# Optimization experiments

Measured on AMD Instinct MI355X. Metric: run time of the kernel, lower is better.

## Reference

```python
import jax, jax.numpy as jnp
import numpy as np

N = 8192      # num nodes
D = 128       # feature dim (input_dim)
E = 262144    # num edges (avg degree 32)
P = 4         # num perspectives (num_pers)
EPSILON = 0.3 # similarity threshold (args.epsilon)


def setup_inputs() -> dict:
    key = jax.random.key(0)
    k1, k2, k3, k4 = jax.random.split(key, 4)
    x = jax.random.normal(k1, (N, D), dtype=jnp.float32)
    ori_index = jax.random.randint(k2, (2, E), 0, N, dtype=jnp.int32)
    ori_weight = jax.random.uniform(k3, (E,), dtype=jnp.float32)
    w_pers = jax.random.normal(k4, (P, D), dtype=jnp.float32)  # weighted-cosine perspective weights
    return {"x": x, "ori_index": ori_index, "ori_weight": ori_weight, "w_pers": w_pers}


def reference(x, ori_index, ori_weight, w_pers):
    n = x.shape[0]
    # to_dense_adj: scatter edge weights into dense [N, N] adjacency (duplicate edges add)
    ori_g = jnp.zeros((n, n), dtype=x.dtype).at[ori_index[0], ori_index[1]].add(ori_weight)

    # GraphLearner (weighted multi-perspective cosine):
    # reweight features per perspective, L2-normalize, cosine sim, mean over perspectives
    xw = x[None, :, :] * w_pers[:, None, :]                              # [P, N, D]
    xn = xw / jnp.maximum(jnp.linalg.norm(xw, axis=-1, keepdims=True), 1e-12)
    sim = jnp.mean(jnp.einsum('pnd,pmd->pnm', xn, xn), axis=0)           # [N, N]
    # epsilon-thresholded learned graph
    sim_g = jnp.where(sim > EPSILON, sim, jnp.zeros_like(sim))

    # purified(sim, ori_g, epsilon): keep original edges where sim*ori_g > epsilon
    pur_g = jnp.where(sim * ori_g > EPSILON, ori_g, jnp.zeros_like(sim))
    new_g = pur_g + sim_g
    # dense_to_sparse has data-dependent output size; return the dense refined
    # adjacency (same information: edges = nonzero(new_g), weights = values).
    return new_g
```

## Files before the change

kernel.cpp:

```cpp
#include <hip/hip_runtime.h>
#include <hip/hip_bf16.h>
#include <stdint.h>

#define N_NODES 8192
#define DIM     128
#define KTOT    512
#define NEDGE   262144
#define EPS     0.3f
#define FIX_DELTA 0.0043f
#define FIX_CAP (1u << 19)
#define LCAP    512
#define HASH_BITS 19
#define HASH_SLOTS (1u << HASH_BITS)

typedef unsigned int u32;
typedef unsigned short u16;
typedef __attribute__((ext_vector_type(8))) short short8;
typedef __attribute__((ext_vector_type(4))) float float4v;

#define OFF_YF  0u
#define OFF_YB  16777216u
#define OFF_CTR 25165824u
#define OFF_HK  25166080u
#define OFF_HV  27263232u
#define OFF_FL  29360384u
#define OFF_UL  31457536u
#define ZERO_VEC4 262160u

__device__ __forceinline__ u16 f2bf(float f) {
    u32 b = __builtin_bit_cast(u32, f);
    b += 0x7fffu + ((b >> 16) & 1u);
    return (u16)(b >> 16);
}

__device__ __forceinline__ float wave_dot(const float* __restrict__ yf,
                                          u32 i, u32 j, int lane) {
    const float4v* ri = (const float4v*)(yf + (size_t)i * KTOT);
    const float4v* rj = (const float4v*)(yf + (size_t)j * KTOT);
    float4v p = ri[lane] * rj[lane] + ri[64 + lane] * rj[64 + lane];
    float s = p.x + p.y + p.z + p.w;
    #pragma unroll
    for (int o = 32; o >= 1; o >>= 1) s += __shfl_xor(s, o, 64);
    return s;
}

__device__ __forceinline__ bool is_edge(const u32* __restrict__ hkey, u32 cell) {
    u32 h = (cell * 2654435761u) >> (32 - HASH_BITS);
    while (true) {
        u32 k = hkey[h];
        if (k == 0u) return false;
        if (k == cell + 1u) return true;
        h = (h + 1u) & (HASH_SLOTS - 1u);
    }
}

__global__ void prep_y(const float* __restrict__ x, const float* __restrict__ wp,
                       float* __restrict__ yf, u16* __restrict__ yb,
                       uint4* __restrict__ zbase) {
    if (blockIdx.x >= 2048) {
        for (u32 idx = (blockIdx.x - 2048) * 256 + threadIdx.x; idx < ZERO_VEC4;
             idx += 512 * 256)
            zbase[idx] = make_uint4(0, 0, 0, 0);
        return;
    }
    int node = blockIdx.x * 4 + (threadIdx.x >> 6);
    int lane = threadIdx.x & 63;
    float x0 = x[node * DIM + lane];
    float x1 = x[node * DIM + lane + 64];
    for (int p = 0; p < 4; ++p) {
        float v0 = x0 * wp[p * DIM + lane];
        float v1 = x1 * wp[p * DIM + lane + 64];
        float ss = v0 * v0 + v1 * v1;
        #pragma unroll
        for (int o = 1; o < 64; o <<= 1) ss += __shfl_xor(ss, o, 64);
        float scale = 0.5f / fmaxf(sqrtf(ss), 1e-12f);
        float y0 = v0 * scale, y1 = v1 * scale;
        int base = node * KTOT + p * DIM;
        yf[base + lane] = y0;       yf[base + lane + 64] = y1;
        yb[base + lane] = f2bf(y0); yb[base + lane + 64] = f2bf(y1);
    }
}

__global__ void edge_insert(const int* __restrict__ idx, const float* __restrict__ w,
                            u32* __restrict__ hkey, float* __restrict__ hval,
                            u32* __restrict__ ucnt, u32* __restrict__ ulist) {
    int e = blockIdx.x * 256 + threadIdx.x;
    u32 cell = (u32)(idx[e] * N_NODES + idx[NEDGE + e]);
    float wv = w[e];
    u32 key = cell + 1u;
    u32 h = (cell * 2654435761u) >> (32 - HASH_BITS);
    while (true) {
        u32 old = atomicCAS(&hkey[h], 0u, key);
        if (old == 0u) { ulist[atomicAdd(ucnt, 1u)] = h; atomicAdd(&hval[h], wv); break; }
        if (old == key) { atomicAdd(&hval[h], wv); break; }
        h = (h + 1u) & (HASH_SLOTS - 1u);
    }
}

#define TM  128
#define BK  64
#define TLD 132

__global__ __launch_bounds__(512)
void gemm_sim(const u16* __restrict__ yb, const float* __restrict__ yf,
              float* __restrict__ out, u32* __restrict__ fcnt, u32* __restrict__ flst) {
    int r = blockIdx.y, c = blockIdx.x;
    int bm, bn;
    if (c < 64 - r) { bm = r;      bn = r + c; }
    else            { bm = 63 - r; bn = bm + (c - (64 - r)); }
    __shared__ __align__(16) char smem[64 * TLD * 4];
    u16* As = (u16*)smem;
    u16* Bs = As + TM * BK;
    float* tbuf = (float*)smem;
    __shared__ u32 s_cnt;
    __shared__ u32 s_list[LCAP];
    int tid = threadIdx.x;
    int lane = tid & 63, wid = tid >> 6;
    int wm = wid >> 1, wn = wid & 1;
    if (tid == 0) s_cnt = 0;

    float4v acc[2][4] = {};
    const u16* arow = yb + (size_t)(bm * TM) * KTOT;
    const u16* brow = yb + (size_t)(bn * TM) * KTOT;

    for (int kt = 0; kt < KTOT / BK; ++kt) {
        __syncthreads();
        #pragma unroll
        for (int q = 0; q < 2; ++q) {
            int cc = q * 512 + wid * 64 + lane;
            int row = cc >> 3;
            int kg = (cc & 7) ^ (row & 7);
            __builtin_amdgcn_global_load_lds(
                (const __attribute__((address_space(1))) void*)(const void*)(arow + (size_t)row * KTOT + kt * BK + kg * 8),
                (__attribute__((address_space(3))) void*)(void*)(As + (q * 512 + wid * 64) * 8),
                16, 0, 0);
            __builtin_amdgcn_global_load_lds(
                (const __attribute__((address_space(1))) void*)(const void*)(brow + (size_t)row * KTOT + kt * BK + kg * 8),
                (__attribute__((address_space(3))) void*)(void*)(Bs + (q * 512 + wid * 64) * 8),
                16, 0, 0);
        }
        __syncthreads();
        #pragma unroll
        for (int kk = 0; kk < 2; ++kk) {
            short8 af[2], bfr[4];
            int kg2 = kk * 4 + (lane >> 4);
            int mrow = wm * 32 + (lane & 15);
            int ncol = wn * 64 + (lane & 15);
            #pragma unroll
            for (int i = 0; i < 2; ++i) {
                int ra = mrow + i * 16;
                af[i] = *(const short8*)&As[ra * BK + ((kg2 ^ (ra & 7)) * 8)];
            }
            #pragma unroll
            for (int j = 0; j < 4; ++j) {
                int rb = ncol + j * 16;
                bfr[j] = *(const short8*)&Bs[rb * BK + ((kg2 ^ (rb & 7)) * 8)];
            }
            #pragma unroll
            for (int i = 0; i < 2; ++i)
                #pragma unroll
                for (int j = 0; j < 4; ++j)
                    acc[i][j] = __builtin_amdgcn_mfma_f32_16x16x32_bf16(
                        af[i], bfr[j], acc[i][j], 0, 0, 0);
        }
    }

    int quad = lane >> 4, lcol = lane & 15;
    #pragma unroll
    for (int i = 0; i < 2; ++i)
        #pragma unroll
        for (int j = 0; j < 4; ++j) {
            int gr0 = bm * TM + wm * 32 + i * 16 + quad * 4;
            int gc  = bn * TM + wn * 64 + j * 16 + lcol;
            #pragma unroll
            for (int rr = 0; rr < 4; ++rr) {
                float s = acc[i][j][rr];
                __builtin_nontemporal_store(s > EPS ? s : 0.f,
                                            &out[(size_t)(gr0 + rr) * N_NODES + gc]);
                if (fabsf(s - EPS) < FIX_DELTA) {
                    u32 cell = (u32)((gr0 + rr) * N_NODES + gc);
                    u32 li = atomicAdd(&s_cnt, 1u);
                    if (li < LCAP) s_list[li] = cell;
                    else { u32 g = atomicAdd(fcnt, 1u); if (g < FIX_CAP) flst[g] = cell; }
                }
            }
        }

    #pragma unroll
    for (int h = 0; h < 2; ++h) {
        __syncthreads();
        if (wn == h) {
            #pragma unroll
            for (int i = 0; i < 2; ++i) {
                int Lr = wm * 32 + i * 16 + quad * 4;
                #pragma unroll
                for (int j = 0; j < 4; ++j) {
                    int Lc = j * 16 + lcol;
                    *(float4v*)&tbuf[Lc * TLD + Lr] = acc[i][j];
                }
            }
        }
        __syncthreads();
        #pragma unroll
        for (int v = 0; v < 4; ++v) {
            int chunk = v * 512 + tid;
            int row = chunk >> 5, c4 = chunk & 31;
            float4v t = *(const float4v*)&tbuf[row * TLD + c4 * 4];
            float4v o;
            #pragma unroll
            for (int rr = 0; rr < 4; ++rr) o[rr] = t[rr] > EPS ? t[rr] : 0.f;
            __builtin_nontemporal_store(o,
                (float4v*)&out[(size_t)(bn * TM + h * 64 + row) * N_NODES + bm * TM + c4 * 4]);
        }
    }

    __syncthreads();
    u32 cnt = s_cnt < LCAP ? s_cnt : LCAP;
    for (u32 t = wid; t < cnt; t += 8) {
        u32 cell = s_list[t];
        u32 ii = cell >> 13, jj = cell & 8191u;
        float s = wave_dot(yf, ii, jj, lane);
        if (lane == 0) {
            float v = s > EPS ? s : 0.f;
            out[(size_t)ii * N_NODES + jj] = v;
            out[(size_t)jj * N_NODES + ii] = v;
        }
    }
}

__global__ void fix_and_edges(const float* __restrict__ yf,
                              const u32* __restrict__ fcnt, const u32* __restrict__ flst,
                              const u32* __restrict__ hkey, const float* __restrict__ hval,
                              const u32* __restrict__ ucnt, const u32* __restrict__ ulist,
                              float* __restrict__ out) {
    int lane = threadIdx.x & 63;
    if (blockIdx.x < 1024) {
        u32 count = *ucnt;
        u32 t = blockIdx.x * 256 + threadIdx.x;
        bool valid = t < count;
        u32 cell = 0; float a = 0.f, sg = 0.f; bool hard = false;
        if (valid) {
            u32 h = ulist[t];
            cell = hkey[h] - 1u;
            a = hval[h];
            sg = out[cell];
            hard = (a > 1.0f) ||
                   (fabsf(sg - EPS) < FIX_DELTA + 1e-6f) ||
                   (sg > 0.f && fabsf(sg * a - EPS) < FIX_DELTA * a + 1e-6f) ||
                   (sg == 0.f && a > 0.9855f);
            if (!hard && sg > 0.f)
                out[cell] = sg + ((sg * a > EPS) ? a : 0.f);
        }
        unsigned long long m = __ballot(hard);
        while (m) {
            int src = __builtin_ctzll(m);
            m &= m - 1;
            u32 cB = __shfl(cell, src, 64);
            float aB = __shfl(a, src, 64);
            float s = wave_dot(yf, cB >> 13, cB & 8191u, lane);
            if (lane == 0) {
                float v = s > EPS ? s : 0.f;
                if (s * aB > EPS) v += aB;
                out[cB] = v;
            }
        }
    } else {
        u32 count = *fcnt; if (count > FIX_CAP) count = FIX_CAP;
        u32 wv = (blockIdx.x - 1024) * 4 + (threadIdx.x >> 6);
        for (u32 t = wv; t < count; t += 64 * 4) {
            u32 cell = flst[t];
            u32 ii = cell >> 13, jj = cell & 8191u;
            float s = wave_dot(yf, ii, jj, lane);
            float v = s > EPS ? s : 0.f;
            u32 mir = jj * (u32)N_NODES + ii;
            if (lane == 0 && !is_edge(hkey, cell)) out[(size_t)ii * N_NODES + jj] = v;
            if (lane == 1 && !is_edge(hkey, mir))  out[(size_t)jj * N_NODES + ii] = v;
        }
    }
}

extern "C" void kernel_launch(void* const* d_in, const int* in_sizes, int n_in,
                              void* d_out, int out_size, void* d_ws, size_t ws_size,
                              hipStream_t stream) {
    const float* x  = (const float*)d_in[0];
    const int*   oi = (const int*)d_in[1];
    const float* ow = (const float*)d_in[2];
    const float* wp = (const float*)d_in[3];
    float* out = (float*)d_out;
    char* ws = (char*)d_ws;
    float* yf = (float*)(ws + OFF_YF);
    u16*   yb = (u16*)(ws + OFF_YB);
    u32*   fc = (u32*)(ws + OFF_CTR);
    u32*   uc = (u32*)(ws + OFF_CTR + 4);
    u32*   hk = (u32*)(ws + OFF_HK);
    float* hv = (float*)(ws + OFF_HV);
    u32*   fl = (u32*)(ws + OFF_FL);
    u32*   ul = (u32*)(ws + OFF_UL);

    prep_y<<<2560, 256, 0, stream>>>(x, wp, yf, yb, (uint4*)(ws + OFF_CTR));
    edge_insert<<<NEDGE / 256, 256, 0, stream>>>(oi, ow, hk, hv, uc, ul);
    gemm_sim<<<dim3(65, 32), 512, 0, stream>>>(yb, yf, out, fc, fl);
    fix_and_edges<<<1088, 256, 0, stream>>>(yf, fc, fl, hk, hv, uc, ul, out);
}
```

Measured before the change: 424.4 us.

## Fuse near-threshold fixes and edge merging into the GEMM epilogue via per-tile edge buckets

Edges are bucketed by the upper-triangular 128x128 tile they fall in during hash insertion, and the GEMM block that owns that tile now applies the edge merge and exact-fp32 recomputes itself. Near-threshold cells are recomputed in-wave through a ballot loop instead of being queued to a global list. This removes the separate fix_and_edges launch and its global fix list. In exchange the GEMM epilogue gets longer, and every block scans the whole overflow list. Edges in the mirrored lower tile must be read after both triangle writes by the same block, which the bucketing by the symmetric tile ensures.

Measured after the change: 429.0 us. Within noise of the previous version (+1.1%).

```diff
diff --git a/kernel.cpp b/kernel.cpp
--- a/kernel.cpp
+++ b/kernel.cpp
@@ -8,10 +8,11 @@
 #define NEDGE   262144
 #define EPS     0.3f
 #define FIX_DELTA 0.0043f
-#define FIX_CAP (1u << 19)
-#define LCAP    512
 #define HASH_BITS 19
 #define HASH_SLOTS (1u << HASH_BITS)
+#define NTRI    2080
+#define TRI_CAP 376
+#define OCAP    131072
 
 typedef unsigned int u32;
 typedef unsigned short u16;
@@ -21,11 +22,12 @@
 #define OFF_YF  0u
 #define OFF_YB  16777216u
 #define OFF_CTR 25165824u
-#define OFF_HK  25166080u
-#define OFF_HV  27263232u
-#define OFF_FL  29360384u
-#define OFF_UL  31457536u
-#define ZERO_VEC4 262160u
+#define OFF_BC  25166080u
+#define OFF_HK  25174528u
+#define OFF_HV  27271680u
+#define OFF_OL  29368832u
+#define OFF_BL  29893120u
+#define ZERO_VEC4 262688u
 
 __device__ __forceinline__ u16 f2bf(float f) {
     u32 b = __builtin_bit_cast(u32, f);
@@ -44,14 +46,10 @@
     return s;
 }
 
-__device__ __forceinline__ bool is_edge(const u32* __restrict__ hkey, u32 cell) {
-    u32 h = (cell * 2654435761u) >> (32 - HASH_BITS);
-    while (true) {
-        u32 k = hkey[h];
-        if (k == 0u) return false;
-        if (k == cell + 1u) return true;
-        h = (h + 1u) & (HASH_SLOTS - 1u);
-    }
+__device__ __forceinline__ u32 tri_of(u32 ti, u32 tj) {
+    u32 bm = ti < tj ? ti : tj;
+    u32 bn = ti < tj ? tj : ti;
+    return bm * (129u - bm) / 2u + (bn - bm);
 }
 
 __global__ void prep_y(const float* __restrict__ x, const float* __restrict__ wp,
@@ -83,15 +81,24 @@
 
 __global__ void edge_insert(const int* __restrict__ idx, const float* __restrict__ w,
                             u32* __restrict__ hkey, float* __restrict__ hval,
-                            u32* __restrict__ ucnt, u32* __restrict__ ulist) {
+                            u32* __restrict__ bcnt, u32* __restrict__ blist,
+                            u32* __restrict__ ocnt, u32* __restrict__ olist) {
     int e = blockIdx.x * 256 + threadIdx.x;
-    u32 cell = (u32)(idx[e] * N_NODES + idx[NEDGE + e]);
+    u32 i = (u32)idx[e], j = (u32)idx[NEDGE + e];
+    u32 cell = i * (u32)N_NODES + j;
     float wv = w[e];
     u32 key = cell + 1u;
     u32 h = (cell * 2654435761u) >> (32 - HASH_BITS);
     while (true) {
         u32 old = atomicCAS(&hkey[h], 0u, key);
-        if (old == 0u) { ulist[atomicAdd(ucnt, 1u)] = h; atomicAdd(&hval[h], wv); break; }
+        if (old == 0u) {
+            u32 tri = tri_of(i >> 7, j >> 7);
+            u32 bi = atomicAdd(&bcnt[tri], 1u);
+            if (bi < TRI_CAP) blist[tri * TRI_CAP + bi] = h;
+            else { u32 g = atomicAdd(ocnt, 1u); if (g < OCAP) olist[g] = h; }
+            atomicAdd(&hval[h], wv);
+            break;
+        }
         if (old == key) { atomicAdd(&hval[h], wv); break; }
         h = (h + 1u) & (HASH_SLOTS - 1u);
     }
@@ -103,7 +110,10 @@
 
 __global__ __launch_bounds__(512)
 void gemm_sim(const u16* __restrict__ yb, const float* __restrict__ yf,
-              float* __restrict__ out, u32* __restrict__ fcnt, u32* __restrict__ flst) {
+              float* __restrict__ out,
+              const u32* __restrict__ hkey, const float* __restrict__ hval,
+              const u32* __restrict__ bcnt, const u32* __restrict__ blist,
+              const u32* __restrict__ ocnt, const u32* __restrict__ olist) {
     int r = blockIdx.y, c = blockIdx.x;
     int bm, bn;
     if (c < 64 - r) { bm = r;      bn = r + c; }
@@ -112,12 +122,9 @@
     u16* As = (u16*)smem;
     u16* Bs = As + TM * BK;
     float* tbuf = (float*)smem;
-    __shared__ u32 s_cnt;
-    __shared__ u32 s_list[LCAP];
     int tid = threadIdx.x;
     int lane = tid & 63, wid = tid >> 6;
     int wm = wid >> 1, wn = wid & 1;
-    if (tid == 0) s_cnt = 0;
 
     float4v acc[2][4] = {};
     const u16* arow = yb + (size_t)(bm * TM) * KTOT;
@@ -177,12 +184,6 @@
                 float s = acc[i][j][rr];
                 __builtin_nontemporal_store(s > EPS ? s : 0.f,
                                             &out[(size_t)(gr0 + rr) * N_NODES + gc]);
-                if (fabsf(s - EPS) < FIX_DELTA) {
-                    u32 cell = (u32)((gr0 + rr) * N_NODES + gc);
-                    u32 li = atomicAdd(&s_cnt, 1u);
-                    if (li < LCAP) s_list[li] = cell;
-                    else { u32 g = atomicAdd(fcnt, 1u); if (g < FIX_CAP) flst[g] = cell; }
-                }
             }
         }
 
@@ -215,66 +216,96 @@
     }
 
     __syncthreads();
-    u32 cnt = s_cnt < LCAP ? s_cnt : LCAP;
-    for (u32 t = wid; t < cnt; t += 8) {
-        u32 cell = s_list[t];
-        u32 ii = cell >> 13, jj = cell & 8191u;
-        float s = wave_dot(yf, ii, jj, lane);
-        if (lane == 0) {
-            float v = s > EPS ? s : 0.f;
-            out[(size_t)ii * N_NODES + jj] = v;
-            out[(size_t)jj * N_NODES + ii] = v;
-        }
-    }
-}
-
-__global__ void fix_and_edges(const float* __restrict__ yf,
-                              const u32* __restrict__ fcnt, const u32* __restrict__ flst,
-                              const u32* __restrict__ hkey, const float* __restrict__ hval,
-                              const u32* __restrict__ ucnt, const u32* __restrict__ ulist,
-                              float* __restrict__ out) {
-    int lane = threadIdx.x & 63;
-    if (blockIdx.x < 1024) {
-        u32 count = *ucnt;
-        u32 t = blockIdx.x * 256 + threadIdx.x;
-        bool valid = t < count;
-        u32 cell = 0; float a = 0.f, sg = 0.f; bool hard = false;
+
+    #pragma unroll
+    for (int i = 0; i < 2; ++i)
+        #pragma unroll
+        for (int j = 0; j < 4; ++j)
+            #pragma unroll
+            for (int rr = 0; rr < 4; ++rr) {
+                float s = acc[i][j][rr];
+                unsigned long long m = __ballot(fabsf(s - EPS) < FIX_DELTA);
+                while (m) {
+                    int src = __builtin_ctzll(m);
+                    m &= m - 1;
+                    u32 ii = (u32)(bm * TM + wm * 32 + i * 16 + (src >> 4) * 4 + rr);
+                    u32 jj = (u32)(bn * TM + wn * 64 + j * 16 + (src & 15));
+                    float sx = wave_dot(yf, ii, jj, lane);
+                    if (lane == 0) {
+                        float v = sx > EPS ? sx : 0.f;
+                        out[(size_t)ii * N_NODES + jj] = v;
+                        out[(size_t)jj * N_NODES + ii] = v;
+                    }
+                }
+            }
+
+    __syncthreads();
+
+    u32 tri = tri_of((u32)bm, (u32)bn);
+    u32 cnt = bcnt[tri]; if (cnt > TRI_CAP) cnt = TRI_CAP;
+    {
+        u32 t = (u32)tid;
+        bool valid = t < cnt;
+        u32 cell = 0; float a = 0.f, sg = 0.f; bool hardc = false;
         if (valid) {
-            u32 h = ulist[t];
+            u32 h = blist[tri * TRI_CAP + t];
             cell = hkey[h] - 1u;
             a = hval[h];
             sg = out[cell];
-            hard = (a > 1.0f) ||
-                   (fabsf(sg - EPS) < FIX_DELTA + 1e-6f) ||
-                   (sg > 0.f && fabsf(sg * a - EPS) < FIX_DELTA * a + 1e-6f) ||
-                   (sg == 0.f && a > 0.9855f);
-            if (!hard && sg > 0.f)
+            hardc = (a > 1.0f) ||
+                    (fabsf(sg - EPS) < FIX_DELTA + 1e-6f) ||
+                    (sg > 0.f && fabsf(sg * a - EPS) < FIX_DELTA * a + 1e-6f) ||
+                    (sg == 0.f && a > 0.9855f);
+            if (!hardc && sg > 0.f)
                 out[cell] = sg + ((sg * a > EPS) ? a : 0.f);
         }
-        unsigned long long m = __ballot(hard);
+        unsigned long long m = __ballot(hardc);
         while (m) {
             int src = __builtin_ctzll(m);
             m &= m - 1;
             u32 cB = __shfl(cell, src, 64);
             float aB = __shfl(a, src, 64);
-            float s = wave_dot(yf, cB >> 13, cB & 8191u, lane);
+            float sx = wave_dot(yf, cB >> 13, cB & 8191u, lane);
             if (lane == 0) {
-                float v = s > EPS ? s : 0.f;
-                if (s * aB > EPS) v += aB;
+                float v = sx > EPS ? sx : 0.f;
+                if (sx * aB > EPS) v += aB;
                 out[cB] = v;
             }
         }
-    } else {
-        u32 count = *fcnt; if (count > FIX_CAP) count = FIX_CAP;
-        u32 wv = (blockIdx.x - 1024) * 4 + (threadIdx.x >> 6);
-        for (u32 t = wv; t < count; t += 64 * 4) {
-            u32 cell = flst[t];
+    }
+
+    u32 ovn = *ocnt; if (ovn > OCAP) ovn = OCAP;
+    for (u32 base = 0; base < ovn; base += 512) {
+        u32 t = base + (u32)tid;
+        bool valid = t < ovn;
+        u32 cell = 0; float a = 0.f, sg = 0.f; bool hardc = false;
+        if (valid) {
+            u32 h = olist[t];
+            cell = hkey[h] - 1u;
             u32 ii = cell >> 13, jj = cell & 8191u;
-            float s = wave_dot(yf, ii, jj, lane);
-            float v = s > EPS ? s : 0.f;
-            u32 mir = jj * (u32)N_NODES + ii;
-            if (lane == 0 && !is_edge(hkey, cell)) out[(size_t)ii * N_NODES + jj] = v;
-            if (lane == 1 && !is_edge(hkey, mir))  out[(size_t)jj * N_NODES + ii] = v;
+            if (tri_of(ii >> 7, jj >> 7) == tri) {
+                a = hval[h];
+                sg = out[cell];
+                hardc = (a > 1.0f) ||
+                        (fabsf(sg - EPS) < FIX_DELTA + 1e-6f) ||
+                        (sg > 0.f && fabsf(sg * a - EPS) < FIX_DELTA * a + 1e-6f) ||
+                        (sg == 0.f && a > 0.9855f);
+                if (!hardc && sg > 0.f)
+                    out[cell] = sg + ((sg * a > EPS) ? a : 0.f);
+            }
+        }
+        unsigned long long m = __ballot(hardc);
+        while (m) {
+            int src = __builtin_ctzll(m);
+            m &= m - 1;
+            u32 cB = __shfl(cell, src, 64);
+            float aB = __shfl(a, src, 64);
+            float sx = wave_dot(yf, cB >> 13, cB & 8191u, lane);
+            if (lane == 0) {
+                float v = sx > EPS ? sx : 0.f;
+                if (sx * aB > EPS) v += aB;
+                out[cB] = v;
+            }
         }
     }
 }
@@ -290,15 +321,14 @@
     char* ws = (char*)d_ws;
     float* yf = (float*)(ws + OFF_YF);
     u16*   yb = (u16*)(ws + OFF_YB);
-    u32*   fc = (u32*)(ws + OFF_CTR);
-    u32*   uc = (u32*)(ws + OFF_CTR + 4);
+    u32*   oc = (u32*)(ws + OFF_CTR);
+    u32*   bc = (u32*)(ws + OFF_BC);
     u32*   hk = (u32*)(ws + OFF_HK);
     float* hv = (float*)(ws + OFF_HV);
-    u32*   fl = (u32*)(ws + OFF_FL);
-    u32*   ul = (u32*)(ws + OFF_UL);
+    u32*   ol = (u32*)(ws + OFF_OL);
+    u32*   bl = (u32*)(ws + OFF_BL);
 
     prep_y<<<2560, 256, 0, stream>>>(x, wp, yf, yb, (uint4*)(ws + OFF_CTR));
-    edge_insert<<<NEDGE / 256, 256, 0, stream>>>(oi, ow, hk, hv, uc, ul);
-    gemm_sim<<<dim3(65, 32), 512, 0, stream>>>(yb, yf, out, fc, fl);
-    fix_and_edges<<<1088, 256, 0, stream>>>(yf, fc, fl, hk, hv, uc, ul, out);
-}
+    edge_insert<<<NEDGE / 256, 256, 0, stream>>>(oi, ow, hk, hv, bc, bl, oc, ol);
+    gemm_sim<<<dim3(65, 32), 512, 0, stream>>>(yb, yf, out, hk, hv, bc, bl, oc, ol);
+}
```
